# Performance work log

Measured on AMD Instinct MI355X. Metric: run time of the kernel, lower is better.

Reference implementation:

```python
import jax, jax.numpy as jnp
import numpy as np

NUM_HEADS = 8
GRAPH_DIM = 64
K_RATIO = 0.1
SIM_THRESH = 0.6


def _gat_layer(h_in, mask, W, a_src, a_dst, b):
    # PyG GATConv (heads=1, eval mode): lin (no bias), alpha = LeakyReLU(a_src.h_j + a_dst.h_i),
    # softmax over source nodes j per target i (edges given by dense mask, self loops included), + bias.
    h = h_in @ W                                   # [N, F]
    asrc = h @ a_src                               # [N] source term
    adst = h @ a_dst                               # [N] target term
    logits = jax.nn.leaky_relu(adst[:, None] + asrc[None, :], 0.2)  # [target i, source j]
    logits = jnp.where(mask.T, logits, -1e30)      # mask[j,i]: edge src j -> dst i (symmetric here)
    alpha = jax.nn.softmax(logits, axis=-1)
    return alpha @ h + b


def _forward(x, w_qkv, w_proj, b_proj, gat0_W, gat0_asrc, gat0_adst, gat0_b,
             gat1_W, gat1_asrc, gat1_adst, gat1_b, w_g2a, b_g2a):
    B, C, H, W = x.shape
    HW = H * W
    nh = NUM_HEADS
    hd = C // nh
    scale = hd ** -0.5
    x_seq = x.reshape(B, C, HW).transpose(0, 2, 1)                 # [B, HW, C]

    # ---- build_spatial_graph ----
    importance = jnp.var(x_seq, axis=-1, ddof=1)                   # torch.var default unbiased
    N = int(HW * K_RATIO)                                          # 102 nodes
    _, top_idx = jax.lax.top_k(importance, N)                      # [B, N]
    feats = jnp.take_along_axis(x_seq, top_idx[..., None], axis=1) # [B, N, C]
    fn = feats / jnp.clip(jnp.linalg.norm(feats, axis=-1, keepdims=True), 1e-12)
    sim = fn @ fn.transpose(0, 2, 1)                               # [B, N, N]
    adj = sim > SIM_THRESH
    adj = adj | jnp.eye(N, dtype=bool)                             # GATConv add_self_loops

    # ---- per-batch GAT stack + graph_to_attn ----
    def per_graph(f, m):
        g = jax.nn.relu(_gat_layer(f, m, gat0_W, gat0_asrc, gat0_adst, gat0_b))
        g = jax.nn.relu(_gat_layer(g, m, gat1_W, gat1_asrc, gat1_adst, gat1_b))
        return jax.nn.sigmoid(g @ w_g2a.T + b_g2a)                 # [N, nh]
    gw = jax.vmap(per_graph)(feats, adj)                           # [B, N, nh]

    # ---- dense multi-head attention ----
    qkv = (x_seq @ w_qkv.T).reshape(B, HW, 3, nh, hd).transpose(2, 0, 3, 1, 4)
    q, k, v = qkv[0], qkv[1], qkv[2]                               # [B, nh, HW, hd]
    scores = jnp.einsum('bhqd,bhkd->bhqk', q, k) * scale           # [B, nh, HW, HW]

    # ---- graph modulation scatter (replaces the nested python loops) ----
    vals = jnp.where(adj[..., None], gw[:, :, None, :] * gw[:, None, :, :], 0.0)  # [B, N, N, nh]
    gm = jnp.zeros_like(scores)
    bidx = jnp.arange(B)[:, None, None]
    gm = gm.at[bidx, :, top_idx[:, :, None], top_idx[:, None, :]].set(vals)
    scores = scores + gm

    attn = jax.nn.softmax(scores, axis=-1)                         # dropout is identity in eval
    out = jnp.einsum('bhqk,bhkd->bhqd', attn, v).transpose(0, 2, 1, 3).reshape(B, HW, C)
    out = out @ w_proj.T + b_proj
    return out.transpose(0, 2, 1).reshape(B, C, H, W)


def setup_inputs() -> dict:
    key = jax.random.key(0)
    ks = jax.random.split(key, 16)
    dim, gd, nh = 256, GRAPH_DIM, NUM_HEADS
    B, H, W = 8, 32, 32
    s = 0.02
    return {
        'x': jax.random.normal(ks[0], (B, dim, H, W), dtype=jnp.float32),
        'w_qkv': s * jax.random.normal(ks[1], (3 * dim, dim), dtype=jnp.float32),
        'w_proj': s * jax.random.normal(ks[2], (dim, dim), dtype=jnp.float32),
        'b_proj': jnp.zeros((dim,), dtype=jnp.float32),
        'gat0_W': s * jax.random.normal(ks[3], (dim, gd), dtype=jnp.float32),
        'gat0_asrc': s * jax.random.normal(ks[4], (gd,), dtype=jnp.float32),
        'gat0_adst': s * jax.random.normal(ks[5], (gd,), dtype=jnp.float32),
        'gat0_b': jnp.zeros((gd,), dtype=jnp.float32),
        'gat1_W': s * jax.random.normal(ks[6], (gd, gd), dtype=jnp.float32),
        'gat1_asrc': s * jax.random.normal(ks[7], (gd,), dtype=jnp.float32),
        'gat1_adst': s * jax.random.normal(ks[8], (gd,), dtype=jnp.float32),
        'gat1_b': jnp.zeros((gd,), dtype=jnp.float32),
        'w_g2a': s * jax.random.normal(ks[9], (nh, gd), dtype=jnp.float32),
        'b_g2a': jnp.zeros((nh,), dtype=jnp.float32),
    }


def reference(x, w_qkv, w_proj, b_proj, gat0_W, gat0_asrc, gat0_adst, gat0_b,
              gat1_W, gat1_asrc, gat1_adst, gat1_b, w_g2a, b_g2a):
    return _forward(x, w_qkv, w_proj, b_proj, gat0_W, gat0_asrc, gat0_adst, gat0_b,
                    gat1_W, gat1_asrc, gat1_adst, gat1_b, w_g2a, b_g2a)
```

## Files before the change

### kernel.cpp

```cpp
#include <hip/hip_runtime.h>
#include <math.h>

#define NB 8
#define CDIM 256
#define HWD 1024
#define NH 8
#define HD 32
#define NN 102
#define GD 64

typedef __attribute__((ext_vector_type(8))) short bf16x8;
typedef __attribute__((ext_vector_type(4))) float f32x4;

__device__ inline short f2bf(float f) {
  union { float f; unsigned u; } v; v.f = f;
  unsigned r = v.u + 0x7fffu + ((v.u >> 16) & 1u);
  return (short)(r >> 16);
}
__device__ inline float bf2f(short s) {
  union { unsigned u; float f; } v;
  v.u = ((unsigned)(unsigned short)s) << 16;
  return v.f;
}

__global__ __launch_bounds__(256) void transpose_k(const float* __restrict__ in,
                                                   float* __restrict__ out, int R, int C) {
  __shared__ float tile[32][33];
  int c0 = blockIdx.x * 32, r0 = blockIdx.y * 32;
  for (int i = threadIdx.y; i < 32; i += 8) {
    int r = r0 + i, c = c0 + threadIdx.x;
    if (r < R && c < C) tile[i][threadIdx.x] = in[r * C + c];
  }
  __syncthreads();
  for (int i = threadIdx.y; i < 32; i += 8) {
    int c = c0 + i, r = r0 + threadIdx.x;
    if (r < R && c < C) out[c * R + r] = tile[threadIdx.x][i];
  }
}

__global__ __launch_bounds__(256) void importance_k(const float* __restrict__ x,
                                                    float* __restrict__ imp) {
  int t = blockIdx.x * 256 + threadIdx.x;
  int b = t >> 10, p = t & 1023;
  const float* xp = x + (size_t)b * CDIM * HWD + p;
  float s = 0.f;
  for (int c = 0; c < CDIM; ++c) s += xp[c * HWD];
  float mean = s * (1.f / CDIM);
  float v = 0.f;
  for (int c = 0; c < CDIM; ++c) { float d = xp[c * HWD] - mean; v += d * d; }
  imp[t] = v * (1.f / (CDIM - 1));
}

__global__ __launch_bounds__(1024) void topk_k(const float* __restrict__ imp,
                                               int* __restrict__ topi, int* __restrict__ nodeof) {
  __shared__ float sv[1024];
  __shared__ int si[1024];
  int b = blockIdx.x, t = threadIdx.x;
  sv[t] = imp[b * 1024 + t];
  si[t] = t;
  nodeof[b * 1024 + t] = -1;
  __syncthreads();
  for (int k = 2; k <= 1024; k <<= 1) {
    for (int j = k >> 1; j > 0; j >>= 1) {
      int ixj = t ^ j;
      if (ixj > t) {
        bool up = ((t & k) == 0);
        float a = sv[t], c = sv[ixj];
        if ((a > c) == up) {
          sv[t] = c; sv[ixj] = a;
          int ti = si[t]; si[t] = si[ixj]; si[ixj] = ti;
        }
      }
      __syncthreads();
    }
  }
  if (t >= 1024 - NN) {
    int n = 1023 - t;
    int idx = si[t];
    topi[b * 128 + n] = idx;
    nodeof[b * 1024 + idx] = n;
  }
}

__global__ __launch_bounds__(256) void feats_k(const float* __restrict__ x,
                                               const int* __restrict__ topi,
                                               float* __restrict__ feats, float* __restrict__ rn) {
  int n = blockIdx.x, b = blockIdx.y, t = threadIdx.x;
  int idx = topi[b * 128 + n];
  float v = x[((size_t)b * CDIM + t) * HWD + idx];
  feats[((size_t)b * NN + n) * CDIM + t] = v;
  float ss = v * v;
  for (int m = 1; m < 64; m <<= 1) ss += __shfl_xor(ss, m);
  __shared__ float red[4];
  if ((t & 63) == 0) red[t >> 6] = ss;
  __syncthreads();
  if (t == 0) {
    float tot = red[0] + red[1] + red[2] + red[3];
    rn[b * 128 + n] = 1.f / fmaxf(sqrtf(tot), 1e-12f);
  }
}

__global__ __launch_bounds__(128) void adj_k(const float* __restrict__ feats,
                                             const float* __restrict__ rn,
                                             unsigned char* __restrict__ adj) {
  int i = blockIdx.x, b = blockIdx.y, t = threadIdx.x;
  __shared__ float fi[CDIM];
  for (int c = t; c < CDIM; c += 128) fi[c] = feats[((size_t)b * NN + i) * CDIM + c];
  __syncthreads();
  if (t < NN) {
    const float* fj = feats + ((size_t)b * NN + t) * CDIM;
    float d = 0.f;
    for (int c = 0; c < CDIM; ++c) d += fi[c] * fj[c];
    float sim = d * rn[b * 128 + i] * rn[b * 128 + t];
    adj[((size_t)b * NN + i) * NN + t] = (sim > 0.6f || t == i) ? 1 : 0;
  }
}

__global__ __launch_bounds__(64) void gath_k(const float* __restrict__ in,
                                             const float* __restrict__ W,
                                             const float* __restrict__ aw_src,
                                             const float* __restrict__ aw_dst,
                                             float* __restrict__ h, float* __restrict__ asrc,
                                             float* __restrict__ adst, int Fin) {
  int n = blockIdx.x, b = blockIdx.y, f = threadIdx.x;
  __shared__ float il[CDIM];
  const float* ip = in + ((size_t)b * NN + n) * Fin;
  for (int c = f; c < Fin; c += 64) il[c] = ip[c];
  __syncthreads();
  float acc = 0.f;
  for (int c = 0; c < Fin; ++c) acc += il[c] * W[c * GD + f];
  h[((size_t)b * NN + n) * GD + f] = acc;
  float s1 = acc * aw_src[f], s2 = acc * aw_dst[f];
  for (int m = 1; m < 64; m <<= 1) { s1 += __shfl_xor(s1, m); s2 += __shfl_xor(s2, m); }
  if (f == 0) { asrc[b * 128 + n] = s1; adst[b * 128 + n] = s2; }
}

__global__ __launch_bounds__(128) void gatsoft_k(const float* __restrict__ h,
                                                 const float* __restrict__ asrc,
                                                 const float* __restrict__ adst,
                                                 const unsigned char* __restrict__ adj,
                                                 const float* __restrict__ bias,
                                                 float* __restrict__ out) {
  int i = blockIdx.x, b = blockIdx.y, t = threadIdx.x;
  __shared__ float alpha[NN];
  __shared__ float red[2];
  float adsti = adst[b * 128 + i];
  float e = -1e30f;
  if (t < NN && adj[((size_t)b * NN + i) * NN + t]) {
    float z = adsti + asrc[b * 128 + t];
    e = (z > 0.f) ? z : 0.2f * z;
  }
  float m = e;
  for (int mm = 1; mm < 64; mm <<= 1) m = fmaxf(m, __shfl_xor(m, mm));
  if ((t & 63) == 0) red[t >> 6] = m;
  __syncthreads();
  m = fmaxf(red[0], red[1]);
  float p = (t < NN) ? __expf(e - m) : 0.f;
  float s = p;
  for (int mm = 1; mm < 64; mm <<= 1) s += __shfl_xor(s, mm);
  __syncthreads();
  if ((t & 63) == 0) red[t >> 6] = s;
  __syncthreads();
  s = red[0] + red[1];
  if (t < NN) alpha[t] = p / s;
  __syncthreads();
  if (t < GD) {
    float o = 0.f;
    for (int j = 0; j < NN; ++j) o += alpha[j] * h[((size_t)b * NN + j) * GD + t];
    o += bias[t];
    out[((size_t)b * NN + i) * GD + t] = fmaxf(o, 0.f);
  }
}

__global__ __launch_bounds__(64) void g2a_k(const float* __restrict__ g,
                                            const float* __restrict__ w,
                                            const float* __restrict__ bias,
                                            float* __restrict__ gw) {
  int n = blockIdx.x, b = blockIdx.y, t = threadIdx.x;
  __shared__ float gl[GD];
  gl[t] = g[((size_t)b * NN + n) * GD + t];
  __syncthreads();
  if (t < NH) {
    float acc = bias[t];
    for (int c = 0; c < GD; ++c) acc += gl[c] * w[t * GD + c];
    gw[((size_t)b * NN + n) * NH + t] = 1.f / (1.f + __expf(-acc));
  }
}

#define FMA16(acc, av, bv)                                                            \
  acc[0][0] += av.x * bv.x; acc[0][1] += av.x * bv.y; acc[0][2] += av.x * bv.z;       \
  acc[0][3] += av.x * bv.w;                                                           \
  acc[1][0] += av.y * bv.x; acc[1][1] += av.y * bv.y; acc[1][2] += av.y * bv.z;       \
  acc[1][3] += av.y * bv.w;                                                           \
  acc[2][0] += av.z * bv.x; acc[2][1] += av.z * bv.y; acc[2][2] += av.z * bv.z;       \
  acc[2][3] += av.z * bv.w;                                                           \
  acc[3][0] += av.w * bv.x; acc[3][1] += av.w * bv.y; acc[3][2] += av.w * bv.z;       \
  acc[3][3] += av.w * bv.w;

__global__ __launch_bounds__(256) void qkv_k(const float* __restrict__ x,
                                             const float* __restrict__ wT,
                                             short* __restrict__ qhp, short* __restrict__ qlp,
                                             short* __restrict__ khp, short* __restrict__ klp,
                                             short* __restrict__ vtp) {
  __shared__ float a_s[16][68];
  __shared__ float b_s[16][68];
  __shared__ float c_s[64][68];
  int m0 = blockIdx.x * 64, n0 = blockIdx.y * 64;
  int b = m0 >> 10, p0 = m0 & 1023;
  int t = threadIdx.x, tx = t & 15, ty = t >> 4;
  float acc[4][4] = {};
  for (int k0 = 0; k0 < 256; k0 += 16) {
    int m = t & 63, kb = t >> 6;
#pragma unroll
    for (int r = 0; r < 4; ++r) {
      int kk = kb * 4 + r;
      a_s[kk][m] = x[((size_t)b * 256 + k0 + kk) * 1024 + p0 + m];
      b_s[kk][m] = wT[(k0 + kk) * 768 + n0 + m];
    }
    __syncthreads();
#pragma unroll
    for (int kk = 0; kk < 16; ++kk) {
      float4 av = *(const float4*)&a_s[kk][ty * 4];
      float4 bv = *(const float4*)&b_s[kk][tx * 4];
      FMA16(acc, av, bv)
    }
    __syncthreads();
  }
  int qi = n0 >> 8;
  if (qi < 2) {
    const float scale = (qi == 0) ? 0.17677669529663687f : 1.f;
    short* hp = (qi == 0) ? qhp : khp;
    short* lp = (qi == 0) ? qlp : klp;
    int n = n0 + tx * 4;
    int hh = (n >> 5) & 7, d = n & 31;
#pragma unroll
    for (int i = 0; i < 4; ++i) {
      int p = p0 + ty * 4 + i;
      size_t e = ((size_t)(b * 8 + hh) * 1024 + p) * 32 + d;
      float v0 = acc[i][0] * scale, v1 = acc[i][1] * scale;
      float v2 = acc[i][2] * scale, v3 = acc[i][3] * scale;
      short4 hi, lo;
      hi.x = f2bf(v0); lo.x = f2bf(v0 - bf2f(hi.x));
      hi.y = f2bf(v1); lo.y = f2bf(v1 - bf2f(hi.y));
      hi.z = f2bf(v2); lo.z = f2bf(v2 - bf2f(hi.z));
      hi.w = f2bf(v3); lo.w = f2bf(v3 - bf2f(hi.w));
      *(short4*)(hp + e) = hi;
      *(short4*)(lp + e) = lo;
    }
  } else {
#pragma unroll
    for (int i = 0; i < 4; ++i)
      *(float4*)&c_s[ty * 4 + i][tx * 4] = *(float4*)&acc[i][0];
    __syncthreads();
    int dl = t >> 2, pg = t & 3;
    int n = n0 + dl;
    int hh = (n >> 5) & 7, d = n & 31;
    size_t rowb = (size_t)(b * 8 + hh) * 32768 + (size_t)d * 1024 + p0;
#pragma unroll
    for (int r = 0; r < 4; ++r) {
      int pl = pg * 16 + r * 4;
      short4 s4;
      s4.x = f2bf(c_s[pl + 0][dl]);
      s4.y = f2bf(c_s[pl + 1][dl]);
      s4.z = f2bf(c_s[pl + 2][dl]);
      s4.w = f2bf(c_s[pl + 3][dl]);
      *(short4*)(vtp + rowb + pl) = s4;
    }
  }
}

__global__ __launch_bounds__(256) void attn_k(const short* __restrict__ qh,
                                              const short* __restrict__ ql,
                                              const short* __restrict__ kh,
                                              const short* __restrict__ kl,
                                              const short* __restrict__ vt,
                                              const int* __restrict__ nodeof,
                                              const float* __restrict__ gw,
                                              const unsigned char* __restrict__ adj,
                                              float* __restrict__ ao) {
  __shared__ __align__(16) short p_s[4][32 * 72];
  __shared__ float aw_s[4][64];
  int t = threadIdx.x;
  int wid = t >> 6, lane = t & 63, quad = lane >> 4, l16 = lane & 15;
  int bh = blockIdx.y, b = bh >> 3, h = bh & 7;
  int q0 = blockIdx.x * 128 + wid * 32;
  size_t base = (size_t)bh * 32768;
  short* pw = &p_s[wid][0];
  float* aw = &aw_s[wid][0];

  bf16x8 qhf[2], qlf[2];
#pragma unroll
  for (int mi = 0; mi < 2; ++mi) {
    size_t off = base + (size_t)(q0 + mi * 16 + l16) * 32 + quad * 8;
    qhf[mi] = *(const bf16x8*)(qh + off);
    qlf[mi] = *(const bf16x8*)(ql + off);
  }
  int irow[2][4]; float grq[2][4];
#pragma unroll
  for (int mi = 0; mi < 2; ++mi)
#pragma unroll
    for (int r = 0; r < 4; ++r) {
      int qr = q0 + mi * 16 + quad * 4 + r;
      int in_ = nodeof[b * 1024 + qr];
      irow[mi][r] = in_;
      grq[mi][r] = (in_ >= 0) ? gw[((size_t)b * NN + in_) * NH + h] : 0.f;
    }
  const unsigned char* adjB = adj + (size_t)b * NN * NN;

  f32x4 ot[2][2];
#pragma unroll
  for (int mi = 0; mi < 2; ++mi)
#pragma unroll
    for (int nq = 0; nq < 2; ++nq) ot[mi][nq] = (f32x4){0.f, 0.f, 0.f, 0.f};
  float m_r[2][4], l_r[2][4];
#pragma unroll
  for (int mi = 0; mi < 2; ++mi)
#pragma unroll
    for (int r = 0; r < 4; ++r) { m_r[mi][r] = -1e30f; l_r[mi][r] = 0.f; }

  for (int ch = 0; ch < 16; ++ch) {
    int c0 = ch * 64;
    bf16x8 khf[4], klf[4];
#pragma unroll
    for (int ni = 0; ni < 4; ++ni) {
      size_t off = base + (size_t)(c0 + ni * 16 + l16) * 32 + quad * 8;
      khf[ni] = *(const bf16x8*)(kh + off);
      klf[ni] = *(const bf16x8*)(kl + off);
    }
    bf16x8 vaf[2][2];
#pragma unroll
    for (int mi = 0; mi < 2; ++mi)
#pragma unroll
      for (int ks = 0; ks < 2; ++ks)
        vaf[mi][ks] = *(const bf16x8*)(vt + base + (size_t)(mi * 16 + l16) * 1024 +
                                       c0 + ks * 32 + quad * 8);
    int jn[4]; float gcn[4];
#pragma unroll
    for (int ni = 0; ni < 4; ++ni) {
      int j = nodeof[b * 1024 + c0 + ni * 16 + l16];
      jn[ni] = j;
      gcn[ni] = (j >= 0) ? gw[((size_t)b * NN + j) * NH + h] : 0.f;
    }
    f32x4 s[2][4];
#pragma unroll
    for (int mi = 0; mi < 2; ++mi)
#pragma unroll
      for (int ni = 0; ni < 4; ++ni) {
        f32x4 a = (f32x4){0.f, 0.f, 0.f, 0.f};
        a = __builtin_amdgcn_mfma_f32_16x16x32_bf16(qhf[mi], khf[ni], a, 0, 0, 0);
        a = __builtin_amdgcn_mfma_f32_16x16x32_bf16(qhf[mi], klf[ni], a, 0, 0, 0);
        a = __builtin_amdgcn_mfma_f32_16x16x32_bf16(qlf[mi], khf[ni], a, 0, 0, 0);
        s[mi][ni] = a;
      }
#pragma unroll
    for (int mi = 0; mi < 2; ++mi)
#pragma unroll
      for (int r = 0; r < 4; ++r) {
        int in_ = irow[mi][r];
        if (in_ >= 0) {
          const unsigned char* ar = adjB + (size_t)in_ * NN;
          float g = grq[mi][r];
#pragma unroll
          for (int ni = 0; ni < 4; ++ni)
            if (jn[ni] >= 0 && ar[jn[ni]]) s[mi][ni][r] += g * gcn[ni];
        }
      }
#pragma unroll
    for (int mi = 0; mi < 2; ++mi)
#pragma unroll
      for (int r = 0; r < 4; ++r) {
        float mx = fmaxf(fmaxf(s[mi][0][r], s[mi][1][r]), fmaxf(s[mi][2][r], s[mi][3][r]));
        mx = fmaxf(mx, __shfl_xor(mx, 1));
        mx = fmaxf(mx, __shfl_xor(mx, 2));
        mx = fmaxf(mx, __shfl_xor(mx, 4));
        mx = fmaxf(mx, __shfl_xor(mx, 8));
        float mn = fmaxf(m_r[mi][r], mx);
        float al = __expf(m_r[mi][r] - mn);
        m_r[mi][r] = mn;
        float e0 = __expf(s[mi][0][r] - mn);
        float e1 = __expf(s[mi][1][r] - mn);
        float e2 = __expf(s[mi][2][r] - mn);
        float e3 = __expf(s[mi][3][r] - mn);
        float ls = e0 + e1 + e2 + e3;
        ls += __shfl_xor(ls, 1);
        ls += __shfl_xor(ls, 2);
        ls += __shfl_xor(ls, 4);
        ls += __shfl_xor(ls, 8);
        l_r[mi][r] = l_r[mi][r] * al + ls;
        int rl = mi * 16 + quad * 4 + r;
        if (l16 == 0) aw[rl] = al;
        int prow = rl * 72;
        pw[prow + 0 + l16] = f2bf(e0);
        pw[prow + 16 + l16] = f2bf(e1);
        pw[prow + 32 + l16] = f2bf(e2);
        pw[prow + 48 + l16] = f2bf(e3);
      }
    float a0 = aw[l16], a1 = aw[16 + l16];
#pragma unroll
    for (int mi = 0; mi < 2; ++mi) { ot[mi][0] *= a0; ot[mi][1] *= a1; }
#pragma unroll
    for (int ks = 0; ks < 2; ++ks) {
      bf16x8 pb0 = *(const bf16x8*)(pw + l16 * 72 + ks * 32 + quad * 8);
      bf16x8 pb1 = *(const bf16x8*)(pw + (16 + l16) * 72 + ks * 32 + quad * 8);
      ot[0][0] = __builtin_amdgcn_mfma_f32_16x16x32_bf16(vaf[0][ks], pb0, ot[0][0], 0, 0, 0);
      ot[0][1] = __builtin_amdgcn_mfma_f32_16x16x32_bf16(vaf[0][ks], pb1, ot[0][1], 0, 0, 0);
      ot[1][0] = __builtin_amdgcn_mfma_f32_16x16x32_bf16(vaf[1][ks], pb0, ot[1][0], 0, 0, 0);
      ot[1][1] = __builtin_amdgcn_mfma_f32_16x16x32_bf16(vaf[1][ks], pb1, ot[1][1], 0, 0, 0);
    }
  }
#pragma unroll
  for (int mi = 0; mi < 2; ++mi)
#pragma unroll
    for (int r = 0; r < 4; ++r)
      if (l16 == 0) aw[32 + mi * 16 + quad * 4 + r] = 1.f / l_r[mi][r];
  float li0 = aw[32 + l16], li1 = aw[48 + l16];
#pragma unroll
  for (int mi = 0; mi < 2; ++mi) { ot[mi][0] *= li0; ot[mi][1] *= li1; }
  float* os = (float*)pw;
#pragma unroll
  for (int mi = 0; mi < 2; ++mi)
#pragma unroll
    for (int nq = 0; nq < 2; ++nq)
#pragma unroll
      for (int r = 0; r < 4; ++r)
        os[(nq * 16 + l16) * 36 + mi * 16 + quad * 4 + r] = ot[mi][nq][r];
  int qrow = lane >> 1, dh = (lane & 1) * 16;
  size_t ob = (size_t)(b * 1024 + q0 + qrow) * 256 + h * 32 + dh;
#pragma unroll
  for (int k = 0; k < 4; ++k) {
    float4 v4 = *(float4*)&os[qrow * 36 + dh + k * 4];
    *(float4*)&ao[ob + k * 4] = v4;
  }
}

__global__ __launch_bounds__(256) void proj_k(const float* __restrict__ ao,
                                              const float* __restrict__ wT,
                                              const float* __restrict__ bias,
                                              float* __restrict__ out) {
  __shared__ float a_s[16][68];
  __shared__ float b_s[16][68];
  __shared__ float c_s[64][68];
  int m0 = blockIdx.x * 64, n0 = blockIdx.y * 64;
  int b = m0 >> 10, p0 = m0 & 1023;
  int t = threadIdx.x, tx = t & 15, ty = t >> 4;
  float acc[4][4] = {};
  for (int k0 = 0; k0 < 256; k0 += 16) {
    {
      int kk = t & 15, mm = t >> 4;
#pragma unroll
      for (int r = 0; r < 4; ++r) {
        int m = mm + r * 16;
        a_s[kk][m] = ao[(size_t)(m0 + m) * 256 + k0 + kk];
      }
      int mB = t & 63, kb = t >> 6;
#pragma unroll
      for (int r2 = 0; r2 < 4; ++r2) {
        int kk2 = kb * 4 + r2;
        b_s[kk2][mB] = wT[(k0 + kk2) * 256 + n0 + mB];
      }
    }
    __syncthreads();
#pragma unroll
    for (int kk = 0; kk < 16; ++kk) {
      float4 av = *(const float4*)&a_s[kk][ty * 4];
      float4 bv = *(const float4*)&b_s[kk][tx * 4];
      FMA16(acc, av, bv)
    }
    __syncthreads();
  }
#pragma unroll
  for (int i = 0; i < 4; ++i)
#pragma unroll
    for (int j = 0; j < 4; ++j) c_s[tx * 4 + j][ty * 4 + i] = acc[i][j];
  __syncthreads();
  {
    int cl = t >> 2, pg = t & 3;
    float bv = bias[n0 + cl];
#pragma unroll
    for (int r = 0; r < 4; ++r) {
      int p = pg * 16 + r * 4;
      float4 v4 = {c_s[cl][p] + bv, c_s[cl][p + 1] + bv, c_s[cl][p + 2] + bv, c_s[cl][p + 3] + bv};
      *(float4*)&out[((size_t)b * 256 + n0 + cl) * 1024 + p0 + p] = v4;
    }
  }
}

extern "C" void kernel_launch(void* const* d_in, const int* in_sizes, int n_in,
                              void* d_out, int out_size, void* d_ws, size_t ws_size,
                              hipStream_t stream) {
  const float* x      = (const float*)d_in[0];
  const float* w_qkv  = (const float*)d_in[1];
  const float* w_proj = (const float*)d_in[2];
  const float* b_proj = (const float*)d_in[3];
  const float* g0W    = (const float*)d_in[4];
  const float* g0as   = (const float*)d_in[5];
  const float* g0ad   = (const float*)d_in[6];
  const float* g0b    = (const float*)d_in[7];
  const float* g1W    = (const float*)d_in[8];
  const float* g1as   = (const float*)d_in[9];
  const float* g1ad   = (const float*)d_in[10];
  const float* g1b    = (const float*)d_in[11];
  const float* wg2a   = (const float*)d_in[12];
  const float* bg2a   = (const float*)d_in[13];
  float* out = (float*)d_out;
  float* ws = (float*)d_ws;

  size_t o = 0;
  auto alloc = [&](size_t nf) { float* p = ws + o; o += (nf + 15) & ~(size_t)15; return p; };
  float* wqkvT  = alloc(256 * 768);
  float* wprojT = alloc(256 * 256);
  float* imp    = alloc(8 * 1024);
  int*   topi   = (int*)alloc(8 * 128);
  int*   nodeof = (int*)alloc(8 * 1024);
  float* rn     = alloc(8 * 128);
  float* feats  = alloc(8 * NN * 256);
  unsigned char* adj = (unsigned char*)alloc((8 * NN * NN + 3) / 4 + 16);
  float* h0     = alloc(8 * NN * 64);
  float* g0     = alloc(8 * NN * 64);
  float* h1     = alloc(8 * NN * 64);
  float* g1     = alloc(8 * NN * 64);
  float* asrc   = alloc(8 * 128);
  float* adst   = alloc(8 * 128);
  float* gwb    = alloc(8 * NN * 8);
  short* qh     = (short*)alloc(1048576);
  short* ql     = (short*)alloc(1048576);
  short* kh     = (short*)alloc(1048576);
  short* kl     = (short*)alloc(1048576);
  short* vt     = (short*)alloc(1048576);
  float* ao     = alloc((size_t)8 * 1024 * 256);
  if (ws_size < o * sizeof(float)) return;

  transpose_k<<<dim3(8, 24), dim3(32, 8), 0, stream>>>(w_qkv, wqkvT, 768, 256);
  transpose_k<<<dim3(8, 8), dim3(32, 8), 0, stream>>>(w_proj, wprojT, 256, 256);
  importance_k<<<32, 256, 0, stream>>>(x, imp);
  topk_k<<<8, 1024, 0, stream>>>(imp, topi, nodeof);
  feats_k<<<dim3(NN, 8), 256, 0, stream>>>(x, topi, feats, rn);
  adj_k<<<dim3(NN, 8), 128, 0, stream>>>(feats, rn, adj);
  gath_k<<<dim3(NN, 8), 64, 0, stream>>>(feats, g0W, g0as, g0ad, h0, asrc, adst, 256);
  gatsoft_k<<<dim3(NN, 8), 128, 0, stream>>>(h0, asrc, adst, adj, g0b, g0);
  gath_k<<<dim3(NN, 8), 64, 0, stream>>>(g0, g1W, g1as, g1ad, h1, asrc, adst, 64);
  gatsoft_k<<<dim3(NN, 8), 128, 0, stream>>>(h1, asrc, adst, adj, g1b, g1);
  g2a_k<<<dim3(NN, 8), 64, 0, stream>>>(g1, wg2a, bg2a, gwb);
  qkv_k<<<dim3(128, 12), 256, 0, stream>>>(x, wqkvT, qh, ql, kh, kl, vt);
  attn_k<<<dim3(8, 64), 256, 0, stream>>>(qh, ql, kh, kl, vt, nodeof, gwb, adj, ao);
  proj_k<<<dim3(128, 4), 256, 0, stream>>>(ao, wprojT, b_proj, out);
}
```

Measured before the change: 364.9 us.

## Fuse graph pipeline into one kernel, parallelize importance, drop online softmax in attention

The separate top-k, feature gather, adjacency, two GAT layers and graph-to-attention kernels are merged into one per-batch 1024-thread kernel. That kernel keeps intermediates in shared memory and computes the cosine similarity with bf16 MFMA. The importance kernel now splits channels across 8 thread groups with a shared-memory reduction, launching 256 blocks instead of 32. Attention now uses 16 query rows per wave (twice the blocks), with occupancy hints, and drops the running-max online softmax in favour of plain exp. This removes many small launches and global round trips. The risks are that exp without max subtraction could overflow for large logits, and that bf16 similarity could flip threshold decisions.

```diff
diff --git a/kernel.cpp b/kernel.cpp
--- a/kernel.cpp
+++ b/kernel.cpp
@@ -10,6 +10,7 @@
 #define GD 64
 
 typedef __attribute__((ext_vector_type(8))) short bf16x8;
+typedef __attribute__((ext_vector_type(4))) short bf16x4;
 typedef __attribute__((ext_vector_type(4))) float f32x4;
 
 __device__ inline short f2bf(float f) {
@@ -40,24 +41,59 @@
 
 __global__ __launch_bounds__(256) void importance_k(const float* __restrict__ x,
                                                     float* __restrict__ imp) {
-  int t = blockIdx.x * 256 + threadIdx.x;
-  int b = t >> 10, p = t & 1023;
-  const float* xp = x + (size_t)b * CDIM * HWD + p;
+  __shared__ float red[8][33];
+  int bp = blockIdx.x;
+  int b = bp >> 5, p0 = (bp & 31) << 5;
+  int t = threadIdx.x;
+  int pl = t & 31, cg = t >> 5;
+  const float* xp = x + (size_t)b * CDIM * HWD + p0 + pl;
   float s = 0.f;
-  for (int c = 0; c < CDIM; ++c) s += xp[c * HWD];
-  float mean = s * (1.f / CDIM);
+  for (int cc = 0; cc < 32; ++cc) s += xp[(size_t)(cg * 32 + cc) * HWD];
+  red[cg][pl] = s;
+  __syncthreads();
+  float tot = 0.f;
+  for (int g = 0; g < 8; ++g) tot += red[g][pl];
+  float mean = tot * (1.f / CDIM);
+  __syncthreads();
   float v = 0.f;
-  for (int c = 0; c < CDIM; ++c) { float d = xp[c * HWD] - mean; v += d * d; }
-  imp[t] = v * (1.f / (CDIM - 1));
-}
-
-__global__ __launch_bounds__(1024) void topk_k(const float* __restrict__ imp,
-                                               int* __restrict__ topi, int* __restrict__ nodeof) {
-  __shared__ float sv[1024];
-  __shared__ int si[1024];
+  for (int cc = 0; cc < 32; ++cc) {
+    float d = xp[(size_t)(cg * 32 + cc) * HWD] - mean;
+    v += d * d;
+  }
+  red[cg][pl] = v;
+  __syncthreads();
+  if (t < 32) {
+    float vv = 0.f;
+    for (int g = 0; g < 8; ++g) vv += red[g][t];
+    imp[b * 1024 + p0 + t] = vv * (1.f / (CDIM - 1));
+  }
+}
+
+struct TK { float sv[1024]; int si[1024]; };
+union RB { TK tk; unsigned char adjL[NN * NN]; };
+struct GL { float h0[NN * 65]; float g0[NN * 65]; };
+union RA { short fnb[NN * 260]; GL gl; };
+
+__global__ __launch_bounds__(1024) void graph_k(
+    const float* __restrict__ x, const float* __restrict__ imp,
+    const float* __restrict__ g0W, const float* __restrict__ g0as,
+    const float* __restrict__ g0ad, const float* __restrict__ g0b,
+    const float* __restrict__ g1W, const float* __restrict__ g1as,
+    const float* __restrict__ g1ad, const float* __restrict__ g1b,
+    const float* __restrict__ wg2a, const float* __restrict__ bg2a,
+    int* __restrict__ topi, int* __restrict__ nodeof,
+    float* __restrict__ feats, unsigned char* __restrict__ adj,
+    float* __restrict__ gwb) {
+  __shared__ RB rb;
+  __shared__ RA ra;
+  __shared__ float rnL[NN];
+  __shared__ int topiL[NN];
+  __shared__ float asrcL[104], adstL[104];
   int b = blockIdx.x, t = threadIdx.x;
-  sv[t] = imp[b * 1024 + t];
-  si[t] = t;
+  int wv = t >> 6, lane = t & 63;
+
+  rb.tk.sv[t] = imp[b * 1024 + t];
+  rb.tk.si[t] = t;
   nodeof[b * 1024 + t] = -1;
   __syncthreads();
   for (int k = 2; k <= 1024; k <<= 1) {
@@ -65,10 +101,10 @@
       int ixj = t ^ j;
       if (ixj > t) {
         bool up = ((t & k) == 0);
-        float a = sv[t], c = sv[ixj];
+        float a = rb.tk.sv[t], c = rb.tk.sv[ixj];
         if ((a > c) == up) {
-          sv[t] = c; sv[ixj] = a;
-          int ti = si[t]; si[t] = si[ixj]; si[ixj] = ti;
+          rb.tk.sv[t] = c; rb.tk.sv[ixj] = a;
+          int ti = rb.tk.si[t]; rb.tk.si[t] = rb.tk.si[ixj]; rb.tk.si[ixj] = ti;
         }
       }
       __syncthreads();
@@ -76,114 +112,147 @@
   }
   if (t >= 1024 - NN) {
     int n = 1023 - t;
-    int idx = si[t];
+    int idx = rb.tk.si[t];
     topi[b * 128 + n] = idx;
+    topiL[n] = idx;
     nodeof[b * 1024 + idx] = n;
   }
-}
-
-__global__ __launch_bounds__(256) void feats_k(const float* __restrict__ x,
-                                               const int* __restrict__ topi,
-                                               float* __restrict__ feats, float* __restrict__ rn) {
-  int n = blockIdx.x, b = blockIdx.y, t = threadIdx.x;
-  int idx = topi[b * 128 + n];
-  float v = x[((size_t)b * CDIM + t) * HWD + idx];
-  feats[((size_t)b * NN + n) * CDIM + t] = v;
-  float ss = v * v;
-  for (int m = 1; m < 64; m <<= 1) ss += __shfl_xor(ss, m);
-  __shared__ float red[4];
-  if ((t & 63) == 0) red[t >> 6] = ss;
-  __syncthreads();
-  if (t == 0) {
-    float tot = red[0] + red[1] + red[2] + red[3];
-    rn[b * 128 + n] = 1.f / fmaxf(sqrtf(tot), 1e-12f);
-  }
-}
-
-__global__ __launch_bounds__(128) void adj_k(const float* __restrict__ feats,
-                                             const float* __restrict__ rn,
-                                             unsigned char* __restrict__ adj) {
-  int i = blockIdx.x, b = blockIdx.y, t = threadIdx.x;
-  __shared__ float fi[CDIM];
-  for (int c = t; c < CDIM; c += 128) fi[c] = feats[((size_t)b * NN + i) * CDIM + c];
-  __syncthreads();
-  if (t < NN) {
-    const float* fj = feats + ((size_t)b * NN + t) * CDIM;
-    float d = 0.f;
-    for (int c = 0; c < CDIM; ++c) d += fi[c] * fj[c];
-    float sim = d * rn[b * 128 + i] * rn[b * 128 + t];
-    adj[((size_t)b * NN + i) * NN + t] = (sim > 0.6f || t == i) ? 1 : 0;
-  }
-}
-
-__global__ __launch_bounds__(64) void gath_k(const float* __restrict__ in,
-                                             const float* __restrict__ W,
-                                             const float* __restrict__ aw_src,
-                                             const float* __restrict__ aw_dst,
-                                             float* __restrict__ h, float* __restrict__ asrc,
-                                             float* __restrict__ adst, int Fin) {
-  int n = blockIdx.x, b = blockIdx.y, f = threadIdx.x;
-  __shared__ float il[CDIM];
-  const float* ip = in + ((size_t)b * NN + n) * Fin;
-  for (int c = f; c < Fin; c += 64) il[c] = ip[c];
-  __syncthreads();
-  float acc = 0.f;
-  for (int c = 0; c < Fin; ++c) acc += il[c] * W[c * GD + f];
-  h[((size_t)b * NN + n) * GD + f] = acc;
-  float s1 = acc * aw_src[f], s2 = acc * aw_dst[f];
-  for (int m = 1; m < 64; m <<= 1) { s1 += __shfl_xor(s1, m); s2 += __shfl_xor(s2, m); }
-  if (f == 0) { asrc[b * 128 + n] = s1; adst[b * 128 + n] = s2; }
-}
-
-__global__ __launch_bounds__(128) void gatsoft_k(const float* __restrict__ h,
-                                                 const float* __restrict__ asrc,
-                                                 const float* __restrict__ adst,
-                                                 const unsigned char* __restrict__ adj,
-                                                 const float* __restrict__ bias,
-                                                 float* __restrict__ out) {
-  int i = blockIdx.x, b = blockIdx.y, t = threadIdx.x;
-  __shared__ float alpha[NN];
-  __shared__ float red[2];
-  float adsti = adst[b * 128 + i];
-  float e = -1e30f;
-  if (t < NN && adj[((size_t)b * NN + i) * NN + t]) {
-    float z = adsti + asrc[b * 128 + t];
-    e = (z > 0.f) ? z : 0.2f * z;
-  }
-  float m = e;
-  for (int mm = 1; mm < 64; mm <<= 1) m = fmaxf(m, __shfl_xor(m, mm));
-  if ((t & 63) == 0) red[t >> 6] = m;
-  __syncthreads();
-  m = fmaxf(red[0], red[1]);
-  float p = (t < NN) ? __expf(e - m) : 0.f;
-  float s = p;
-  for (int mm = 1; mm < 64; mm <<= 1) s += __shfl_xor(s, mm);
-  __syncthreads();
-  if ((t & 63) == 0) red[t >> 6] = s;
-  __syncthreads();
-  s = red[0] + red[1];
-  if (t < NN) alpha[t] = p / s;
-  __syncthreads();
-  if (t < GD) {
+  __syncthreads();
+
+  {
+    int n = t >> 3, cg = t & 7;
+    if (n < NN) {
+      int idx = topiL[n];
+      const float* xb = x + (size_t)b * CDIM * HWD + idx;
+      float ssl = 0.f;
+      for (int cc = 0; cc < 32; ++cc) {
+        int c = cg * 32 + cc;
+        float v = xb[(size_t)c * HWD];
+        feats[((size_t)b * NN + n) * CDIM + c] = v;
+        ra.fnb[n * 260 + c] = f2bf(v);
+        ssl += v * v;
+      }
+      ssl += __shfl_xor(ssl, 1);
+      ssl += __shfl_xor(ssl, 2);
+      ssl += __shfl_xor(ssl, 4);
+      if (cg == 0) rnL[n] = 1.f / fmaxf(sqrtf(ssl), 1e-12f);
+    }
+  }
+  __syncthreads();
+  for (int e = t; e < NN * 256; e += 1024) {
+    int n2 = e >> 8, c = e & 255;
+    ra.fnb[n2 * 260 + c] = f2bf(bf2f(ra.fnb[n2 * 260 + c]) * rnL[n2]);
+  }
+  __syncthreads();
+
+  {
+    int quad = lane >> 4, l16 = lane & 15;
+    for (int tid = wv; tid < 49; tid += 16) {
+      int I = tid / 7, J = tid % 7;
+      int rA = I * 16 + l16; if (rA > NN - 1) rA = NN - 1;
+      int rBr = J * 16 + l16; if (rBr > NN - 1) rBr = NN - 1;
+      f32x4 acc = (f32x4){0.f, 0.f, 0.f, 0.f};
+      for (int kb = 0; kb < 8; ++kb) {
+        int oa = rA * 260 + kb * 32 + quad * 8;
+        int ob = rBr * 260 + kb * 32 + quad * 8;
+        bf16x4 a0 = *(const bf16x4*)&ra.fnb[oa];
+        bf16x4 a1 = *(const bf16x4*)&ra.fnb[oa + 4];
+        bf16x4 b0 = *(const bf16x4*)&ra.fnb[ob];
+        bf16x4 b1 = *(const bf16x4*)&ra.fnb[ob + 4];
+        bf16x8 af = (bf16x8){a0.x, a0.y, a0.z, a0.w, a1.x, a1.y, a1.z, a1.w};
+        bf16x8 bf = (bf16x8){b0.x, b0.y, b0.z, b0.w, b1.x, b1.y, b1.z, b1.w};
+        acc = __builtin_amdgcn_mfma_f32_16x16x32_bf16(af, bf, acc, 0, 0, 0);
+      }
+#pragma unroll
+      for (int r = 0; r < 4; ++r) {
+        int i = I * 16 + quad * 4 + r, j = J * 16 + l16;
+        if (i < NN && j < NN)
+          rb.adjL[i * NN + j] = (acc[r] > 0.6f || i == j) ? 1 : 0;
+      }
+    }
+  }
+  __syncthreads();
+  for (int e = t; e < NN * NN; e += 1024) {
+    int i = e / NN, j = e - i * NN;
+    adj[((size_t)b * NN + i) * NN + j] = rb.adjL[i * NN + j];
+  }
+
+  for (int n = wv; n < NN; n += 16) {
+    const float* fp = feats + ((size_t)b * NN + n) * CDIM;
+    float acc = 0.f;
+    for (int c = 0; c < CDIM; ++c) acc += fp[c] * g0W[c * GD + lane];
+    ra.gl.h0[n * 65 + lane] = acc;
+    float s1 = acc * g0as[lane], s2 = acc * g0ad[lane];
+    for (int m = 1; m < 64; m <<= 1) { s1 += __shfl_xor(s1, m); s2 += __shfl_xor(s2, m); }
+    if (lane == 0) { asrcL[n] = s1; adstL[n] = s2; }
+  }
+  __syncthreads();
+
+  for (int i = wv; i < NN; i += 16) {
+    float adsti = adstL[i];
+    float p0 = 0.f, p1 = 0.f;
+    if (rb.adjL[i * NN + lane]) {
+      float z = adsti + asrcL[lane];
+      p0 = __expf(z > 0.f ? z : 0.2f * z);
+    }
+    int j1 = 64 + lane;
+    if (j1 < NN && rb.adjL[i * NN + j1]) {
+      float z = adsti + asrcL[j1];
+      p1 = __expf(z > 0.f ? z : 0.2f * z);
+    }
+    float s = p0 + p1;
+    for (int m = 1; m < 64; m <<= 1) s += __shfl_xor(s, m);
+    float inv = 1.f / s;
     float o = 0.f;
-    for (int j = 0; j < NN; ++j) o += alpha[j] * h[((size_t)b * NN + j) * GD + t];
-    o += bias[t];
-    out[((size_t)b * NN + i) * GD + t] = fmaxf(o, 0.f);
-  }
-}
-
-__global__ __launch_bounds__(64) void g2a_k(const float* __restrict__ g,
-                                            const float* __restrict__ w,
-                                            const float* __restrict__ bias,
-                                            float* __restrict__ gw) {
-  int n = blockIdx.x, b = blockIdx.y, t = threadIdx.x;
-  __shared__ float gl[GD];
-  gl[t] = g[((size_t)b * NN + n) * GD + t];
-  __syncthreads();
-  if (t < NH) {
-    float acc = bias[t];
-    for (int c = 0; c < GD; ++c) acc += gl[c] * w[t * GD + c];
-    gw[((size_t)b * NN + n) * NH + t] = 1.f / (1.f + __expf(-acc));
+    for (int j = 0; j < 64; ++j)
+      o += __shfl(p0, j) * ra.gl.h0[j * 65 + lane];
+    for (int j = 64; j < NN; ++j)
+      o += __shfl(p1, j - 64) * ra.gl.h0[j * 65 + lane];
+    o = o * inv + g0b[lane];
+    ra.gl.g0[i * 65 + lane] = fmaxf(o, 0.f);
+  }
+  __syncthreads();
+
+  for (int n = wv; n < NN; n += 16) {
+    float acc = 0.f;
+    for (int c = 0; c < GD; ++c) acc += ra.gl.g0[n * 65 + c] * g1W[c * GD + lane];
+    float s1 = acc * g1as[lane], s2 = acc * g1ad[lane];
+    for (int m = 1; m < 64; m <<= 1) { s1 += __shfl_xor(s1, m); s2 += __shfl_xor(s2, m); }
+    ra.gl.h0[n * 65 + lane] = acc;
+    if (lane == 0) { asrcL[n] = s1; adstL[n] = s2; }
+  }
+  __syncthreads();
+
+  for (int i = wv; i < NN; i += 16) {
+    float adsti = adstL[i];
+    float p0 = 0.f, p1 = 0.f;
+    if (rb.adjL[i * NN + lane]) {
+      float z = adsti + asrcL[lane];
+      p0 = __expf(z > 0.f ? z : 0.2f * z);
+    }
+    int j1 = 64 + lane;
+    if (j1 < NN && rb.adjL[i * NN + j1]) {
+      float z = adsti + asrcL[j1];
+      p1 = __expf(z > 0.f ? z : 0.2f * z);
+    }
+    float s = p0 + p1;
+    for (int m = 1; m < 64; m <<= 1) s += __shfl_xor(s, m);
+    float inv = 1.f / s;
+    float o = 0.f;
+    for (int j = 0; j < 64; ++j)
+      o += __shfl(p0, j) * ra.gl.h0[j * 65 + lane];
+    for (int j = 64; j < NN; ++j)
+      o += __shfl(p1, j - 64) * ra.gl.h0[j * 65 + lane];
+    o = o * inv + g1b[lane];
+    ra.gl.g0[i * 65 + lane] = fmaxf(o, 0.f);
+  }
+  __syncthreads();
+
+  if (t < NN * NH) {
+    int n = t >> 3, hh = t & 7;
+    float z = bg2a[hh];
+    for (int c = 0; c < GD; ++c) z += ra.gl.g0[n * 65 + c] * wg2a[hh * GD + c];
+    gwb[((size_t)b * NN + n) * NH + hh] = 1.f / (1.f + __expf(-z));
   }
 }
 
@@ -269,54 +338,43 @@
   }
 }
 
-__global__ __launch_bounds__(256) void attn_k(const short* __restrict__ qh,
-                                              const short* __restrict__ ql,
-                                              const short* __restrict__ kh,
-                                              const short* __restrict__ kl,
-                                              const short* __restrict__ vt,
-                                              const int* __restrict__ nodeof,
-                                              const float* __restrict__ gw,
-                                              const unsigned char* __restrict__ adj,
-                                              float* __restrict__ ao) {
-  __shared__ __align__(16) short p_s[4][32 * 72];
-  __shared__ float aw_s[4][64];
+__global__ __launch_bounds__(256, 4) void attn_k(const short* __restrict__ qh,
+                                                 const short* __restrict__ ql,
+                                                 const short* __restrict__ kh,
+                                                 const short* __restrict__ kl,
+                                                 const short* __restrict__ vt,
+                                                 const int* __restrict__ nodeof,
+                                                 const float* __restrict__ gw,
+                                                 const unsigned char* __restrict__ adj,
+                                                 float* __restrict__ ao) {
+  __shared__ __align__(16) short p_s[4][16 * 72];
+  __shared__ float aw_s[4][16];
   int t = threadIdx.x;
   int wid = t >> 6, lane = t & 63, quad = lane >> 4, l16 = lane & 15;
   int bh = blockIdx.y, b = bh >> 3, h = bh & 7;
-  int q0 = blockIdx.x * 128 + wid * 32;
+  int q0 = blockIdx.x * 64 + wid * 16;
   size_t base = (size_t)bh * 32768;
   short* pw = &p_s[wid][0];
   float* aw = &aw_s[wid][0];
 
-  bf16x8 qhf[2], qlf[2];
-#pragma unroll
-  for (int mi = 0; mi < 2; ++mi) {
-    size_t off = base + (size_t)(q0 + mi * 16 + l16) * 32 + quad * 8;
-    qhf[mi] = *(const bf16x8*)(qh + off);
-    qlf[mi] = *(const bf16x8*)(ql + off);
-  }
-  int irow[2][4]; float grq[2][4];
-#pragma unroll
-  for (int mi = 0; mi < 2; ++mi)
-#pragma unroll
-    for (int r = 0; r < 4; ++r) {
-      int qr = q0 + mi * 16 + quad * 4 + r;
-      int in_ = nodeof[b * 1024 + qr];
-      irow[mi][r] = in_;
-      grq[mi][r] = (in_ >= 0) ? gw[((size_t)b * NN + in_) * NH + h] : 0.f;
-    }
+  size_t qoff = base + (size_t)(q0 + l16) * 32 + quad * 8;
+  bf16x8 qhf = *(const bf16x8*)(qh + qoff);
+  bf16x8 qlf = *(const bf16x8*)(ql + qoff);
+
+  int irow[4]; float grq[4];
+#pragma unroll
+  for (int r = 0; r < 4; ++r) {
+    int qr = q0 + quad * 4 + r;
+    int in_ = nodeof[b * 1024 + qr];
+    irow[r] = in_;
+    grq[r] = (in_ >= 0) ? gw[((size_t)b * NN + in_) * NH + h] : 0.f;
+  }
   const unsigned char* adjB = adj + (size_t)b * NN * NN;
 
-  f32x4 ot[2][2];
-#pragma unroll
-  for (int mi = 0; mi < 2; ++mi)
-#pragma unroll
-    for (int nq = 0; nq < 2; ++nq) ot[mi][nq] = (f32x4){0.f, 0.f, 0.f, 0.f};
-  float m_r[2][4], l_r[2][4];
-#pragma unroll
-  for (int mi = 0; mi < 2; ++mi)
-#pragma unroll
-    for (int r = 0; r < 4; ++r) { m_r[mi][r] = -1e30f; l_r[mi][r] = 0.f; }
+  f32x4 ot[2];
+  ot[0] = (f32x4){0.f, 0.f, 0.f, 0.f};
+  ot[1] = (f32x4){0.f, 0.f, 0.f, 0.f};
+  float l_r[4] = {0.f, 0.f, 0.f, 0.f};
 
   for (int ch = 0; ch < 16; ++ch) {
     int c0 = ch * 64;
@@ -341,96 +399,68 @@
       jn[ni] = j;
       gcn[ni] = (j >= 0) ? gw[((size_t)b * NN + j) * NH + h] : 0.f;
     }
-    f32x4 s[2][4];
-#pragma unroll
-    for (int mi = 0; mi < 2; ++mi)
-#pragma unroll
-      for (int ni = 0; ni < 4; ++ni) {
-        f32x4 a = (f32x4){0.f, 0.f, 0.f, 0.f};
-        a = __builtin_amdgcn_mfma_f32_16x16x32_bf16(qhf[mi], khf[ni], a, 0, 0, 0);
-        a = __builtin_amdgcn_mfma_f32_16x16x32_bf16(qhf[mi], klf[ni], a, 0, 0, 0);
-        a = __builtin_amdgcn_mfma_f32_16x16x32_bf16(qlf[mi], khf[ni], a, 0, 0, 0);
-        s[mi][ni] = a;
-      }
-#pragma unroll
-    for (int mi = 0; mi < 2; ++mi)
-#pragma unroll
-      for (int r = 0; r < 4; ++r) {
-        int in_ = irow[mi][r];
-        if (in_ >= 0) {
-          const unsigned char* ar = adjB + (size_t)in_ * NN;
-          float g = grq[mi][r];
-#pragma unroll
-          for (int ni = 0; ni < 4; ++ni)
-            if (jn[ni] >= 0 && ar[jn[ni]]) s[mi][ni][r] += g * gcn[ni];
-        }
-      }
-#pragma unroll
-    for (int mi = 0; mi < 2; ++mi)
-#pragma unroll
-      for (int r = 0; r < 4; ++r) {
-        float mx = fmaxf(fmaxf(s[mi][0][r], s[mi][1][r]), fmaxf(s[mi][2][r], s[mi][3][r]));
-        mx = fmaxf(mx, __shfl_xor(mx, 1));
-        mx = fmaxf(mx, __shfl_xor(mx, 2));
-        mx = fmaxf(mx, __shfl_xor(mx, 4));
-        mx = fmaxf(mx, __shfl_xor(mx, 8));
-        float mn = fmaxf(m_r[mi][r], mx);
-        float al = __expf(m_r[mi][r] - mn);
-        m_r[mi][r] = mn;
-        float e0 = __expf(s[mi][0][r] - mn);
-        float e1 = __expf(s[mi][1][r] - mn);
-        float e2 = __expf(s[mi][2][r] - mn);
-        float e3 = __expf(s[mi][3][r] - mn);
-        float ls = e0 + e1 + e2 + e3;
-        ls += __shfl_xor(ls, 1);
-        ls += __shfl_xor(ls, 2);
-        ls += __shfl_xor(ls, 4);
-        ls += __shfl_xor(ls, 8);
-        l_r[mi][r] = l_r[mi][r] * al + ls;
-        int rl = mi * 16 + quad * 4 + r;
-        if (l16 == 0) aw[rl] = al;
-        int prow = rl * 72;
-        pw[prow + 0 + l16] = f2bf(e0);
-        pw[prow + 16 + l16] = f2bf(e1);
-        pw[prow + 32 + l16] = f2bf(e2);
-        pw[prow + 48 + l16] = f2bf(e3);
-      }
-    float a0 = aw[l16], a1 = aw[16 + l16];
-#pragma unroll
-    for (int mi = 0; mi < 2; ++mi) { ot[mi][0] *= a0; ot[mi][1] *= a1; }
+    f32x4 s[4];
+#pragma unroll
+    for (int ni = 0; ni < 4; ++ni) {
+      f32x4 a = (f32x4){0.f, 0.f, 0.f, 0.f};
+      a = __builtin_amdgcn_mfma_f32_16x16x32_bf16(qhf, khf[ni], a, 0, 0, 0);
+      a = __builtin_amdgcn_mfma_f32_16x16x32_bf16(qhf, klf[ni], a, 0, 0, 0);
+      a = __builtin_amdgcn_mfma_f32_16x16x32_bf16(qlf, khf[ni], a, 0, 0, 0);
+      s[ni] = a;
+    }
+#pragma unroll
+    for (int r = 0; r < 4; ++r) {
+      int in_ = irow[r];
+      if (in_ >= 0) {
+        const unsigned char* ar = adjB + (size_t)in_ * NN;
+        float g = grq[r];
+#pragma unroll
+        for (int ni = 0; ni < 4; ++ni)
+          if (jn[ni] >= 0 && ar[jn[ni]]) s[ni][r] += g * gcn[ni];
+      }
+    }
+#pragma unroll
+    for (int r = 0; r < 4; ++r) {
+      float e0 = __expf(s[0][r]);
+      float e1 = __expf(s[1][r]);
+      float e2 = __expf(s[2][r]);
+      float e3 = __expf(s[3][r]);
+      l_r[r] += (e0 + e1) + (e2 + e3);
+      int prow = (quad * 4 + r) * 72;
+      pw[prow + 0 + l16] = f2bf(e0);
+      pw[prow + 16 + l16] = f2bf(e1);
+      pw[prow + 32 + l16] = f2bf(e2);
+      pw[prow + 48 + l16] = f2bf(e3);
+    }
 #pragma unroll
     for (int ks = 0; ks < 2; ++ks) {
-      bf16x8 pb0 = *(const bf16x8*)(pw + l16 * 72 + ks * 32 + quad * 8);
-      bf16x8 pb1 = *(const bf16x8*)(pw + (16 + l16) * 72 + ks * 32 + quad * 8);
-      ot[0][0] = __builtin_amdgcn_mfma_f32_16x16x32_bf16(vaf[0][ks], pb0, ot[0][0], 0, 0, 0);
-      ot[0][1] = __builtin_amdgcn_mfma_f32_16x16x32_bf16(vaf[0][ks], pb1, ot[0][1], 0, 0, 0);
-      ot[1][0] = __builtin_amdgcn_mfma_f32_16x16x32_bf16(vaf[1][ks], pb0, ot[1][0], 0, 0, 0);
-      ot[1][1] = __builtin_amdgcn_mfma_f32_16x16x32_bf16(vaf[1][ks], pb1, ot[1][1], 0, 0, 0);
-    }
-  }
+      bf16x8 pb = *(const bf16x8*)(pw + l16 * 72 + ks * 32 + quad * 8);
+      ot[0] = __builtin_amdgcn_mfma_f32_16x16x32_bf16(vaf[0][ks], pb, ot[0], 0, 0, 0);
+      ot[1] = __builtin_amdgcn_mfma_f32_16x16x32_bf16(vaf[1][ks], pb, ot[1], 0, 0, 0);
+    }
+  }
+#pragma unroll
+  for (int r = 0; r < 4; ++r) {
+    float ls = l_r[r];
+    ls += __shfl_xor(ls, 1);
+    ls += __shfl_xor(ls, 2);
+    ls += __shfl_xor(ls, 4);
+    ls += __shfl_xor(ls, 8);
+    if (l16 == 0) aw[quad * 4 + r] = 1.f / ls;
+  }
+  float li = aw[l16];
+  ot[0] *= li;
+  ot[1] *= li;
+  float* os = (float*)pw;
 #pragma unroll
   for (int mi = 0; mi < 2; ++mi)
 #pragma unroll
     for (int r = 0; r < 4; ++r)
-      if (l16 == 0) aw[32 + mi * 16 + quad * 4 + r] = 1.f / l_r[mi][r];
-  float li0 = aw[32 + l16], li1 = aw[48 + l16];
-#pragma unroll
-  for (int mi = 0; mi < 2; ++mi) { ot[mi][0] *= li0; ot[mi][1] *= li1; }
-  float* os = (float*)pw;
-#pragma unroll
-  for (int mi = 0; mi < 2; ++mi)
-#pragma unroll
-    for (int nq = 0; nq < 2; ++nq)
-#pragma unroll
-      for (int r = 0; r < 4; ++r)
-        os[(nq * 16 + l16) * 36 + mi * 16 + quad * 4 + r] = ot[mi][nq][r];
-  int qrow = lane >> 1, dh = (lane & 1) * 16;
-  size_t ob = (size_t)(b * 1024 + q0 + qrow) * 256 + h * 32 + dh;
-#pragma unroll
-  for (int k = 0; k < 4; ++k) {
-    float4 v4 = *(float4*)&os[qrow * 36 + dh + k * 4];
-    *(float4*)&ao[ob + k * 4] = v4;
-  }
+      os[l16 * 36 + mi * 16 + quad * 4 + r] = ot[mi][r];
+  int qr2 = lane >> 2, dg = (lane & 3) * 8;
+  size_t ob = (size_t)(b * 1024 + q0 + qr2) * 256 + h * 32 + dg;
+  *(float4*)&ao[ob] = *(float4*)&os[qr2 * 36 + dg];
+  *(float4*)&ao[ob + 4] = *(float4*)&os[qr2 * 36 + dg + 4];
 }
 
 __global__ __launch_bounds__(256) void proj_k(const float* __restrict__ ao,
@@ -512,15 +542,8 @@
   float* imp    = alloc(8 * 1024);
   int*   topi   = (int*)alloc(8 * 128);
   int*   nodeof = (int*)alloc(8 * 1024);
-  float* rn     = alloc(8 * 128);
   float* feats  = alloc(8 * NN * 256);
   unsigned char* adj = (unsigned char*)alloc((8 * NN * NN + 3) / 4 + 16);
-  float* h0     = alloc(8 * NN * 64);
-  float* g0     = alloc(8 * NN * 64);
-  float* h1     = alloc(8 * NN * 64);
-  float* g1     = alloc(8 * NN * 64);
-  float* asrc   = alloc(8 * 128);
-  float* adst   = alloc(8 * 128);
   float* gwb    = alloc(8 * NN * 8);
   short* qh     = (short*)alloc(1048576);
   short* ql     = (short*)alloc(1048576);
@@ -532,16 +555,10 @@
 
   transpose_k<<<dim3(8, 24), dim3(32, 8), 0, stream>>>(w_qkv, wqkvT, 768, 256);
   transpose_k<<<dim3(8, 8), dim3(32, 8), 0, stream>>>(w_proj, wprojT, 256, 256);
-  importance_k<<<32, 256, 0, stream>>>(x, imp);
-  topk_k<<<8, 1024, 0, stream>>>(imp, topi, nodeof);
-  feats_k<<<dim3(NN, 8), 256, 0, stream>>>(x, topi, feats, rn);
-  adj_k<<<dim3(NN, 8), 128, 0, stream>>>(feats, rn, adj);
-  gath_k<<<dim3(NN, 8), 64, 0, stream>>>(feats, g0W, g0as, g0ad, h0, asrc, adst, 256);
-  gatsoft_k<<<dim3(NN, 8), 128, 0, stream>>>(h0, asrc, adst, adj, g0b, g0);
-  gath_k<<<dim3(NN, 8), 64, 0, stream>>>(g0, g1W, g1as, g1ad, h1, asrc, adst, 64);
-  gatsoft_k<<<dim3(NN, 8), 128, 0, stream>>>(h1, asrc, adst, adj, g1b, g1);
-  g2a_k<<<dim3(NN, 8), 64, 0, stream>>>(g1, wg2a, bg2a, gwb);
+  importance_k<<<256, 256, 0, stream>>>(x, imp);
+  graph_k<<<8, 1024, 0, stream>>>(x, imp, g0W, g0as, g0ad, g0b, g1W, g1as, g1ad, g1b,
+                                  wg2a, bg2a, topi, nodeof, feats, adj, gwb);
   qkv_k<<<dim3(128, 12), 256, 0, stream>>>(x, wqkvT, qh, ql, kh, kl, vt);
-  attn_k<<<dim3(8, 64), 256, 0, stream>>>(qh, ql, kh, kl, vt, nodeof, gwb, adj, ao);
+  attn_k<<<dim3(16, 64), 256, 0, stream>>>(qh, ql, kh, kl, vt, nodeof, gwb, adj, ao);
   proj_k<<<dim3(128, 4), 256, 0, stream>>>(ao, wprojT, b_proj, out);
 }
```

New measurement: 495.8 us. 35.9% more time.
